# Kernel tuning notes

Hardware: AMD Instinct MI355X
Metric: run time of the kernel (lower is better)

Reference implementation:

```python
import jax, jax.numpy as jnp
import numpy as np

B, T, D, R, DFF = 4, 4096, 1024, 128, 4096
WINDOW = 1024
EPS = 1e-6


def rmsnorm(x, w):
    x32 = x.astype(jnp.float32)
    rms = jax.lax.rsqrt(jnp.mean(x32 * x32, axis=-1, keepdims=True) + EPS)
    return (x32 * rms).astype(x.dtype) * w


def rope(x, cos, sin):
    # x: (B, T, R); cos/sin: (T, R//2)
    d = x.shape[-1] // 2
    x1, x2 = x[..., :d], x[..., d:]
    return jnp.concatenate([x1 * cos + x2 * sin, -x1 * sin + x2 * cos], axis=-1)


def setup_inputs() -> dict:
    key = jax.random.key(0)
    ks = jax.random.split(key, 12)
    s = 0.02  # realistic weight scale
    return {
        "x": jax.random.normal(ks[0], (B, T, D), jnp.float32),
        "Uq": jax.random.normal(ks[1], (R, D), jnp.float32) * s,
        "Uk": jax.random.normal(ks[2], (R, D), jnp.float32) * s,
        "Uv": jax.random.normal(ks[3], (R, D), jnp.float32) * s,
        "cos": jnp.cos(jnp.outer(jnp.arange(T, dtype=jnp.float32),
                                 1.0 / (10000.0 ** (jnp.arange(R // 2, dtype=jnp.float32) / (R // 2))))),
        "sin": jnp.sin(jnp.outer(jnp.arange(T, dtype=jnp.float32),
                                 1.0 / (10000.0 ** (jnp.arange(R // 2, dtype=jnp.float32) / (R // 2))))),
        "ln1_w": jnp.ones((D,), jnp.float32),
        "ln2_w": jnp.ones((D,), jnp.float32),
        "Wo": jax.random.normal(ks[4], (D, R), jnp.float32) * s,
        "w1": jax.random.normal(ks[5], (DFF, D), jnp.float32) * s,
        "w3": jax.random.normal(ks[6], (DFF, D), jnp.float32) * s,
        "w2": jax.random.normal(ks[7], (D, DFF), jnp.float32) * s,
        "window_size": WINDOW,
    }


def reference(x, Uq, Uk, Uv, cos, sin, ln1_w, ln2_w, Wo, w1, w3, w2, window_size):
    Bx, Tx, _ = x.shape
    rank = Uq.shape[0]
    normed = rmsnorm(x, ln1_w)
    q = rope(normed @ Uq.T, cos, sin)  # (B, T, R)
    k = rope(normed @ Uk.T, cos, sin)
    v = normed @ Uv.T
    # windowed causal single-head SDPA
    scale = 1.0 / jnp.sqrt(jnp.float32(rank))
    scores = jnp.einsum("btr,bsr->bts", q, k) * scale  # (B, T, T)
    row = jnp.arange(Tx)[:, None]
    col = jnp.arange(Tx)[None, :]
    mask = (col <= row) & ((row - col) <= window_size)
    scores = jnp.where(mask, scores, jnp.float32(-jnp.inf))
    attn = jax.nn.softmax(scores, axis=-1)
    y = jnp.einsum("bts,bsr->btr", attn, v)  # (B, T, R)
    x = x + y @ Wo.T
    h = rmsnorm(x, ln2_w)
    ffn = ((h @ w1.T) * jax.nn.silu(h @ w3.T)) @ w2.T
    return x + ffn
```

## Files before the change

kernel.cpp:

```cpp
#include <hip/hip_runtime.h>
#include <hip/hip_bf16.h>
#include <stdint.h>

#define BT   16384
#define TT   4096
#define NB   4
#define DD   1024
#define RR   128
#define DFFC 4096

typedef __bf16 bf16_8 __attribute__((ext_vector_type(8)));
typedef float  f32x4  __attribute__((ext_vector_type(4)));

__device__ __forceinline__ void async16(const void* g, void* l) {
  __builtin_amdgcn_global_load_lds((__attribute__((address_space(1))) void*)(g),
                                   (__attribute__((address_space(3))) void*)(l),
                                   16, 0, 0);
}

__global__ __launch_bounds__(256) void cvt_k(const float* __restrict__ src,
                                             __hip_bfloat16* __restrict__ dst, int n4) {
  const int i = blockIdx.x * 256 + threadIdx.x;
  if (i >= n4) return;
  const float4 v = ((const float4*)src)[i];
  __hip_bfloat16* o = dst + (size_t)i * 4;
  o[0] = __float2bfloat16(v.x);
  o[1] = __float2bfloat16(v.y);
  o[2] = __float2bfloat16(v.z);
  o[3] = __float2bfloat16(v.w);
}

__global__ __launch_bounds__(256) void rmsnorm_k(const float* __restrict__ x,
                                                 const float* __restrict__ wgt,
                                                 __hip_bfloat16* __restrict__ out) {
  const int row = blockIdx.x;
  const int t = threadIdx.x;
  const float4 v = ((const float4*)(x + (size_t)row * DD))[t];
  float ss = v.x*v.x + v.y*v.y + v.z*v.z + v.w*v.w;
  #pragma unroll
  for (int m = 1; m < 64; m <<= 1) ss += __shfl_xor(ss, m, 64);
  __shared__ float red[4];
  if ((t & 63) == 0) red[t >> 6] = ss;
  __syncthreads();
  ss = red[0] + red[1] + red[2] + red[3];
  const float rms = rsqrtf(ss * (1.0f / DD) + 1e-6f);
  const float4 wv = ((const float4*)wgt)[t];
  __hip_bfloat16* o = out + (size_t)row * DD + t * 4;
  o[0] = __float2bfloat16(v.x * rms * wv.x);
  o[1] = __float2bfloat16(v.y * rms * wv.y);
  o[2] = __float2bfloat16(v.z * rms * wv.z);
  o[3] = __float2bfloat16(v.w * rms * wv.w);
}

__global__ __launch_bounds__(256) void rope_k(const __hip_bfloat16* __restrict__ qkv,
                                              const float* __restrict__ cosb,
                                              const float* __restrict__ sinb,
                                              __hip_bfloat16* __restrict__ qr,
                                              __hip_bfloat16* __restrict__ kr) {
  const int idx = blockIdx.x * 256 + threadIdx.x;
  const int row = idx >> 6;
  const int i = idx & 63;
  const int tpos = row & (TT - 1);
  const float c = cosb[tpos * 64 + i];
  const float s = sinb[tpos * 64 + i];
  const size_t base = (size_t)row * 384;
  const float q1 = __bfloat162float(qkv[base + i]);
  const float q2 = __bfloat162float(qkv[base + 64 + i]);
  const float k1 = __bfloat162float(qkv[base + 128 + i]);
  const float k2 = __bfloat162float(qkv[base + 192 + i]);
  const size_t ob = (size_t)row * 128;
  qr[ob + i]      = __float2bfloat16( q1 * c + q2 * s);
  qr[ob + 64 + i] = __float2bfloat16(-q1 * s + q2 * c);
  kr[ob + i]      = __float2bfloat16( k1 * c + k2 * s);
  kr[ob + 64 + i] = __float2bfloat16(-k1 * s + k2 * c);
}

__global__ __launch_bounds__(256) void vtrans_k(const __hip_bfloat16* __restrict__ qkv,
                                                __hip_bfloat16* __restrict__ Vt) {
  const int b = blockIdx.y, t0 = blockIdx.x * 64, t = threadIdx.x;
  #pragma unroll
  for (int i = 0; i < 4; ++i) {
    const int flat8 = i * 256 + t;
    const int row = flat8 >> 4;
    const int d8 = (flat8 & 15) * 8;
    const bf16_8 v = *(const bf16_8*)&qkv[((size_t)(b * TT + t0 + row)) * 384 + 256 + d8];
    #pragma unroll
    for (int j = 0; j < 8; ++j)
      ((__bf16*)Vt)[((size_t)(b * 128 + d8 + j)) * TT + t0 + row] = v[j];
  }
}

enum { EPI_BF16 = 0, EPI_RESID = 1, EPI_GATE = 2 };

template <int EPI>
__global__ __launch_bounds__(256) void gemm_bt(
    const __hip_bfloat16* __restrict__ A,
    const __hip_bfloat16* __restrict__ Bw,
    const float* __restrict__ resid,
    const __hip_bfloat16* __restrict__ gate,
    __hip_bfloat16* __restrict__ outb,
    float* __restrict__ outf,
    int N, int K) {
  __shared__ __hip_bfloat16 As[128 * 64];
  __shared__ __hip_bfloat16 Bs[128 * 64];
  const int t = threadIdx.x;
  const int w = t >> 6, lane = t & 63;
  const int wm = w >> 1, wn = w & 1;
  const int quad = lane >> 4, l16 = lane & 15;
  const int m0 = blockIdx.y * 128, n0 = blockIdx.x * 128;

  const __hip_bfloat16* Ab = A + (size_t)m0 * K;
  const __hip_bfloat16* Bb = Bw + (size_t)n0 * K;

  const int rloc = w * 8 + (lane >> 3);
  const int c0 = (((lane & 7) ^ ((lane >> 3) & 7)) << 3);
  const int swz = (l16 & 7);

  f32x4 acc[4][4] = {};

  for (int k0 = 0; k0 < K; k0 += 64) {
    #pragma unroll
    for (int j = 0; j < 4; ++j) {
      async16(Ab + (size_t)(j * 32 + rloc) * K + k0 + c0, &As[j * 2048 + w * 512]);
      async16(Bb + (size_t)(j * 32 + rloc) * K + k0 + c0, &Bs[j * 2048 + w * 512]);
    }
    __syncthreads();
    #pragma unroll
    for (int kc = 0; kc < 2; ++kc) {
      bf16_8 af[4], bfr[4];
      #pragma unroll
      for (int i = 0; i < 4; ++i) {
        const int pos = (((kc * 4 + quad) ^ swz) << 3);
        af[i]  = *(const bf16_8*)&As[(wm * 64 + i * 16 + l16) * 64 + pos];
        bfr[i] = *(const bf16_8*)&Bs[(wn * 64 + i * 16 + l16) * 64 + pos];
      }
      #pragma unroll
      for (int mt = 0; mt < 4; ++mt) {
        #pragma unroll
        for (int nt = 0; nt < 4; ++nt)
          acc[mt][nt] = __builtin_amdgcn_mfma_f32_16x16x32_bf16(af[mt], bfr[nt], acc[mt][nt], 0, 0, 0);
      }
    }
    __syncthreads();
  }

  #pragma unroll
  for (int mt = 0; mt < 4; ++mt) {
    #pragma unroll
    for (int nt = 0; nt < 4; ++nt) {
      #pragma unroll
      for (int r = 0; r < 4; ++r) {
        const int row = m0 + wm * 64 + mt * 16 + quad * 4 + r;
        const int col = n0 + wn * 64 + nt * 16 + l16;
        const size_t idx = (size_t)row * N + col;
        const float v = acc[mt][nt][r];
        if (EPI == EPI_BF16) {
          outb[idx] = __float2bfloat16(v);
        } else if (EPI == EPI_RESID) {
          outf[idx] = resid[idx] + v;
        } else {
          const float sv = v / (1.0f + __expf(-v));
          outb[idx] = __float2bfloat16(__bfloat162float(gate[idx]) * sv);
        }
      }
    }
  }
}

__global__ __launch_bounds__(256) void attn_k(const __hip_bfloat16* __restrict__ qr,
                                              const __hip_bfloat16* __restrict__ kr,
                                              const __hip_bfloat16* __restrict__ Vt,
                                              __hip_bfloat16* __restrict__ y,
                                              const int* __restrict__ winp) {
  __shared__ __hip_bfloat16 Ksm[64 * 128];
  __shared__ __hip_bfloat16 Vsm[128 * 64];
  __shared__ __hip_bfloat16 Psm[4 * 16 * 72];
  const int t = threadIdx.x, w = t >> 6, lane = t & 63;
  const int quad = lane >> 4, l16 = lane & 15;
  const int b = blockIdx.y, t0 = blockIdx.x * 64;
  const int tw0 = t0 + w * 16;
  const int win = *winp;
  int kb_lo = t0 - win;
  if (kb_lo < 0) kb_lo = 0;
  kb_lo &= ~63;

  bf16_8 qf[4];
  const __hip_bfloat16* qb = qr + ((size_t)(b * TT + tw0 + l16)) * 128 + quad * 8;
  #pragma unroll
  for (int kk = 0; kk < 4; ++kk) qf[kk] = *(const bf16_8*)(qb + kk * 32);

  f32x4 o[8] = {};
  float mrow[4] = {-1e30f, -1e30f, -1e30f, -1e30f};
  float lrow[4] = {0.f, 0.f, 0.f, 0.f};
  const float scale = 0.08838834764831845f;

  const int krow_loc = (w * 4) + (lane >> 4);
  const int kc = ((lane & 15) ^ (krow_loc & 15)) << 3;
  const int vloc = lane >> 3;
  const int vc = ((lane & 7) ^ vloc) << 3;

  for (int kb0 = kb_lo; kb0 <= t0; kb0 += 64) {
    const __hip_bfloat16* kbp = kr + ((size_t)(b * TT + kb0)) * 128;
    #pragma unroll
    for (int i = 0; i < 4; ++i) {
      const int krow = i * 16 + krow_loc;
      async16(kbp + (size_t)krow * 128 + kc, &Ksm[i * 2048 + w * 512]);
    }
    #pragma unroll
    for (int i = 0; i < 4; ++i) {
      const int d0 = (i * 4 + w) * 8;
      const int dr = d0 + vloc;
      async16(Vt + ((size_t)(b * 128 + dr)) * TT + kb0 + vc, &Vsm[d0 * 64]);
    }
    __syncthreads();

    f32x4 s[4] = {};
    #pragma unroll
    for (int kk = 0; kk < 4; ++kk) {
      #pragma unroll
      for (int nt = 0; nt < 4; ++nt) {
        const int cc = ((kk * 4 + quad) ^ l16) << 3;
        const bf16_8 bfrag = *(const bf16_8*)&Ksm[(nt * 16 + l16) * 128 + cc];
        s[nt] = __builtin_amdgcn_mfma_f32_16x16x32_bf16(qf[kk], bfrag, s[nt], 0, 0, 0);
      }
    }

    float mb[4] = {-1e30f, -1e30f, -1e30f, -1e30f};
    #pragma unroll
    for (int nt = 0; nt < 4; ++nt) {
      #pragma unroll
      for (int r = 0; r < 4; ++r) {
        const int tq = tw0 + quad * 4 + r;
        const int scol = kb0 + nt * 16 + l16;
        float v = s[nt][r] * scale;
        const bool ok = (scol <= tq) && (tq - scol <= win);
        v = ok ? v : -1e30f;
        s[nt][r] = v;
        mb[r] = fmaxf(mb[r], v);
      }
    }

    #pragma unroll
    for (int r = 0; r < 4; ++r) {
      float m = mb[r];
      m = fmaxf(m, __shfl_xor(m, 1, 16));
      m = fmaxf(m, __shfl_xor(m, 2, 16));
      m = fmaxf(m, __shfl_xor(m, 4, 16));
      m = fmaxf(m, __shfl_xor(m, 8, 16));
      const float mn = fmaxf(mrow[r], m);
      const float alpha = __expf(mrow[r] - mn);
      mrow[r] = mn;
      float rs = 0.f;
      #pragma unroll
      for (int nt = 0; nt < 4; ++nt) {
        const float pv = __expf(s[nt][r] - mn);
        s[nt][r] = pv;
        rs += pv;
      }
      rs += __shfl_xor(rs, 1, 16);
      rs += __shfl_xor(rs, 2, 16);
      rs += __shfl_xor(rs, 4, 16);
      rs += __shfl_xor(rs, 8, 16);
      lrow[r] = lrow[r] * alpha + rs;
      #pragma unroll
      for (int n2 = 0; n2 < 8; ++n2) o[n2][r] *= alpha;
    }

    __hip_bfloat16* pw = &Psm[w * 1152];
    #pragma unroll
    for (int nt = 0; nt < 4; ++nt) {
      #pragma unroll
      for (int r = 0; r < 4; ++r)
        pw[(quad * 4 + r) * 72 + nt * 16 + l16] = __float2bfloat16(s[nt][r]);
    }
    asm volatile("s_waitcnt lgkmcnt(0)" ::: "memory");

    #pragma unroll
    for (int kk2 = 0; kk2 < 2; ++kk2) {
      const bf16_8 pa = *(const bf16_8*)&Psm[w * 1152 + l16 * 72 + kk2 * 32 + quad * 8];
      #pragma unroll
      for (int n2 = 0; n2 < 8; ++n2) {
        const int cc = ((kk2 * 4 + quad) ^ (l16 & 7)) << 3;
        const bf16_8 vb = *(const bf16_8*)&Vsm[(n2 * 16 + l16) * 64 + cc];
        o[n2] = __builtin_amdgcn_mfma_f32_16x16x32_bf16(pa, vb, o[n2], 0, 0, 0);
      }
    }
    __syncthreads();
  }

  #pragma unroll
  for (int n2 = 0; n2 < 8; ++n2) {
    #pragma unroll
    for (int r = 0; r < 4; ++r) {
      const int row = b * TT + tw0 + quad * 4 + r;
      const int col = n2 * 16 + l16;
      y[(size_t)row * 128 + col] = __float2bfloat16(o[n2][r] / lrow[r]);
    }
  }
}

extern "C" void kernel_launch(void* const* d_in, const int* in_sizes, int n_in,
                              void* d_out, int out_size, void* d_ws, size_t ws_size,
                              hipStream_t stream) {
  const float* x    = (const float*)d_in[0];
  const float* Uq   = (const float*)d_in[1];
  const float* Uk   = (const float*)d_in[2];
  const float* Uv   = (const float*)d_in[3];
  const float* cosb = (const float*)d_in[4];
  const float* sinb = (const float*)d_in[5];
  const float* ln1  = (const float*)d_in[6];
  const float* ln2  = (const float*)d_in[7];
  const float* Wo   = (const float*)d_in[8];
  const float* w1   = (const float*)d_in[9];
  const float* w3   = (const float*)d_in[10];
  const float* w2   = (const float*)d_in[11];
  const int*   winp = (const int*)d_in[12];
  float* out = (float*)d_out;

  uint8_t* p = (uint8_t*)d_ws;
  auto take = [&](size_t bytes) {
    uint8_t* q = p;
    p += (bytes + 255) & ~(size_t)255;
    return q;
  };

  __hip_bfloat16* h1     = (__hip_bfloat16*)take((size_t)BT * DFFC * 2);
  __hip_bfloat16* gb     = h1;
  __hip_bfloat16* normed = (__hip_bfloat16*)take((size_t)BT * DD * 2);
  __hip_bfloat16* hb     = normed;
  __hip_bfloat16* qkv    = (__hip_bfloat16*)take((size_t)BT * 384 * 2);
  __hip_bfloat16* yb     = qkv;
  __hip_bfloat16* qr_    = (__hip_bfloat16*)take((size_t)BT * RR * 2);
  __hip_bfloat16* kr_    = (__hip_bfloat16*)take((size_t)BT * RR * 2);
  __hip_bfloat16* Vt     = (__hip_bfloat16*)take((size_t)BT * RR * 2);
  __hip_bfloat16* Ucat   = (__hip_bfloat16*)take((size_t)384 * DD * 2);
  __hip_bfloat16* Wob    = (__hip_bfloat16*)take((size_t)DD * RR * 2);
  __hip_bfloat16* W1b    = (__hip_bfloat16*)take((size_t)DFFC * DD * 2);
  __hip_bfloat16* W3b    = (__hip_bfloat16*)take((size_t)DFFC * DD * 2);
  __hip_bfloat16* W2b    = (__hip_bfloat16*)take((size_t)DD * DFFC * 2);
  float* x_mid = out;

  cvt_k<<<128, 256, 0, stream>>>(Uq, Ucat, RR * DD / 4);
  cvt_k<<<128, 256, 0, stream>>>(Uk, Ucat + (size_t)RR * DD, RR * DD / 4);
  cvt_k<<<128, 256, 0, stream>>>(Uv, Ucat + (size_t)2 * RR * DD, RR * DD / 4);
  cvt_k<<<128, 256, 0, stream>>>(Wo, Wob, DD * RR / 4);
  cvt_k<<<4096, 256, 0, stream>>>(w1, W1b, DFFC * DD / 4);
  cvt_k<<<4096, 256, 0, stream>>>(w3, W3b, DFFC * DD / 4);
  cvt_k<<<4096, 256, 0, stream>>>(w2, W2b, DD * DFFC / 4);

  rmsnorm_k<<<BT, 256, 0, stream>>>(x, ln1, normed);

  gemm_bt<EPI_BF16><<<dim3(3, 128), 256, 0, stream>>>(normed, Ucat, nullptr, nullptr,
                                                      qkv, nullptr, 384, DD);

  rope_k<<<BT * 64 / 256, 256, 0, stream>>>(qkv, cosb, sinb, qr_, kr_);
  vtrans_k<<<dim3(TT / 64, NB), 256, 0, stream>>>(qkv, Vt);

  attn_k<<<dim3(TT / 64, NB), 256, 0, stream>>>(qr_, kr_, Vt, yb, winp);

  gemm_bt<EPI_RESID><<<dim3(8, 128), 256, 0, stream>>>(yb, Wob, x, nullptr,
                                                       nullptr, x_mid, DD, RR);

  rmsnorm_k<<<BT, 256, 0, stream>>>(x_mid, ln2, hb);

  gemm_bt<EPI_BF16><<<dim3(32, 128), 256, 0, stream>>>(hb, W1b, nullptr, nullptr,
                                                       h1, nullptr, DFFC, DD);
  gemm_bt<EPI_GATE><<<dim3(32, 128), 256, 0, stream>>>(hb, W3b, nullptr, h1,
                                                       gb, nullptr, DFFC, DD);
  gemm_bt<EPI_RESID><<<dim3(8, 128), 256, 0, stream>>>(gb, W2b, x_mid, nullptr,
                                                       nullptr, out, DD, DFFC);
}
```

Before: 845.8 us.

## Add 256x256-tile pipelined GEMM kernel for the FFN matmuls

Adds a new 512-thread GEMM kernel with 256x256 output tiles, double-buffered async global-to-LDS loads that are interleaved with MFMA quarter-steps, XOR-swizzled LDS layout, raised wave priority during MFMA, and an XCD-aware block remapping. The three FFN GEMMs now use it in place of the 128x128 kernel. The aim is higher data reuse per tile and better overlap of loads with matrix math on the largest matmuls. In exchange it needs 128 KB of LDS per block and many accumulator registers, which limits occupancy. Its correctness depends on the dimensions dividing evenly by 256.

```diff
diff --git a/kernel.cpp b/kernel.cpp
--- a/kernel.cpp
+++ b/kernel.cpp
@@ -167,6 +167,130 @@
   }
 }
 
+#define G256_BAR()  asm volatile("s_barrier" ::: "memory")
+#define G256_VMW4() asm volatile("s_waitcnt vmcnt(4)" ::: "memory")
+#define G256_VMW0() asm volatile("s_waitcnt vmcnt(0)" ::: "memory")
+
+#define G256_DSA(mh_) \
+  { _Pragma("unroll") for (int mt = 0; mt < 4; ++mt) { \
+      const int rb_ = (rbA + (mh_) * 64 + mt * 16) * 64; \
+      a[mt][0] = *(const bf16_8*)&Ac[rb_ + p0]; \
+      a[mt][1] = *(const bf16_8*)&Ac[rb_ + p1]; } }
+
+#define G256_DSB(nh_) \
+  { _Pragma("unroll") for (int nt = 0; nt < 2; ++nt) { \
+      const int rb_ = (rbB + (nh_) * 32 + nt * 16) * 64; \
+      b[nt][0] = *(const bf16_8*)&Bc[rb_ + p0]; \
+      b[nt][1] = *(const bf16_8*)&Bc[rb_ + p1]; } }
+
+#define G256_MMA(mh_, nh_) \
+  { __builtin_amdgcn_s_setprio(1); \
+    _Pragma("unroll") for (int kk = 0; kk < 2; ++kk) \
+      _Pragma("unroll") for (int mt = 0; mt < 4; ++mt) \
+        _Pragma("unroll") for (int nt = 0; nt < 2; ++nt) \
+          acc[(mh_) * 4 + mt][(nh_) * 2 + nt] = __builtin_amdgcn_mfma_f32_16x16x32_bf16( \
+              a[mt][kk], b[nt][kk], acc[(mh_) * 4 + mt][(nh_) * 2 + nt], 0, 0, 0); \
+    __builtin_amdgcn_s_setprio(0); }
+
+#define G256_TILE(CUR, kt_) { \
+    const __hip_bfloat16* Ac = As[CUR]; \
+    const __hip_bfloat16* Bc = Bs[CUR]; \
+    const int nb_ = (CUR) ^ 1; \
+    const bool pf = ((kt_) + 1) < NT; \
+    const int kn = ((kt_) + 1) << 6; \
+    if (!pf) { G256_VMW0(); G256_BAR(); } \
+    G256_DSA(0); G256_DSB(0); if (pf) { stageA(0, nb_, kn); } \
+    G256_BAR(); G256_MMA(0, 0); G256_VMW4(); G256_BAR(); \
+    G256_DSB(1); if (pf) { stageB(0, nb_, kn); } \
+    G256_BAR(); G256_MMA(0, 1); G256_VMW4(); G256_BAR(); \
+    G256_DSA(1); if (pf) { stageB(1, nb_, kn); } \
+    G256_BAR(); G256_MMA(1, 1); G256_VMW4(); G256_BAR(); \
+    G256_DSB(0); if (pf) { stageA(1, nb_, kn); } \
+    G256_BAR(); G256_MMA(1, 0); G256_VMW4(); G256_BAR(); \
+  }
+
+template <int EPI>
+__global__ __launch_bounds__(512, 2) void gemm256(
+    const __hip_bfloat16* __restrict__ A,
+    const __hip_bfloat16* __restrict__ Bw,
+    const float* __restrict__ resid,
+    const __hip_bfloat16* __restrict__ gate,
+    __hip_bfloat16* __restrict__ outb,
+    float* __restrict__ outf,
+    int N, int K) {
+  __shared__ __hip_bfloat16 As[2][256 * 64];
+  __shared__ __hip_bfloat16 Bs[2][256 * 64];
+  const int t = threadIdx.x;
+  const int w = t >> 6, lane = t & 63;
+  const int wm = w >> 2, wn = w & 3;
+  const int quad = lane >> 4, l16 = lane & 15;
+
+  const int gx = gridDim.x;
+  const int nwg = gx * gridDim.y;
+  int lin = blockIdx.y * gx + blockIdx.x;
+  lin = (lin & 7) * (nwg >> 3) + (lin >> 3);
+  const int m0 = (lin / gx) * 256;
+  const int n0 = (lin % gx) * 256;
+
+  const __hip_bfloat16* Ab = A + (size_t)m0 * K;
+  const __hip_bfloat16* Bb = Bw + (size_t)n0 * K;
+
+  const int rl = lane >> 3;
+  const int c0 = (((lane & 7) ^ rl) << 3);
+
+  auto stageA = [&](int h, int buf, int k0) {
+    const int r0 = h * 64 + (w << 3);
+    async16(Ab + (size_t)(r0 + rl) * K + k0 + c0, &As[buf][r0 * 64]);
+    const int r1 = r0 + 128;
+    async16(Ab + (size_t)(r1 + rl) * K + k0 + c0, &As[buf][r1 * 64]);
+  };
+  auto stageB = [&](int h, int buf, int k0) {
+    const int s0 = (w >> 2) * 64 + h * 32 + (w & 3) * 8;
+    async16(Bb + (size_t)(s0 + rl) * K + k0 + c0, &Bs[buf][s0 * 64]);
+    const int s1 = s0 + 128;
+    async16(Bb + (size_t)(s1 + rl) * K + k0 + c0, &Bs[buf][s1 * 64]);
+  };
+
+  const int rbA = wm * 128 + l16;
+  const int rbB = wn * 64 + l16;
+  const int p0 = ((quad ^ (l16 & 7)) << 3);
+  const int p1 = (((4 + quad) ^ (l16 & 7)) << 3);
+
+  f32x4 acc[8][4] = {};
+  bf16_8 a[4][2], b[2][2];
+  const int NT = K >> 6;
+
+  stageA(0, 0, 0); stageB(0, 0, 0); stageB(1, 0, 0); stageA(1, 0, 0);
+  G256_VMW4(); G256_BAR();
+
+  for (int kt = 0; kt < NT; kt += 2) {
+    G256_TILE(0, kt);
+    G256_TILE(1, kt + 1);
+  }
+
+  #pragma unroll
+  for (int mf = 0; mf < 8; ++mf) {
+    #pragma unroll
+    for (int nf = 0; nf < 4; ++nf) {
+      #pragma unroll
+      for (int r = 0; r < 4; ++r) {
+        const int row = m0 + wm * 128 + mf * 16 + quad * 4 + r;
+        const int col = n0 + wn * 64 + nf * 16 + l16;
+        const size_t idx = (size_t)row * N + col;
+        const float v = acc[mf][nf][r];
+        if (EPI == EPI_BF16) {
+          outb[idx] = __float2bfloat16(v);
+        } else if (EPI == EPI_RESID) {
+          outf[idx] = resid[idx] + v;
+        } else {
+          const float sv = v / (1.0f + __expf(-v));
+          outb[idx] = __float2bfloat16(__bfloat162float(gate[idx]) * sv);
+        }
+      }
+    }
+  }
+}
+
 __global__ __launch_bounds__(256) void attn_k(const __hip_bfloat16* __restrict__ qr,
                                               const __hip_bfloat16* __restrict__ kr,
                                               const __hip_bfloat16* __restrict__ Vt,
@@ -363,10 +487,10 @@
 
   rmsnorm_k<<<BT, 256, 0, stream>>>(x_mid, ln2, hb);
 
-  gemm_bt<EPI_BF16><<<dim3(32, 128), 256, 0, stream>>>(hb, W1b, nullptr, nullptr,
-                                                       h1, nullptr, DFFC, DD);
-  gemm_bt<EPI_GATE><<<dim3(32, 128), 256, 0, stream>>>(hb, W3b, nullptr, h1,
-                                                       gb, nullptr, DFFC, DD);
-  gemm_bt<EPI_RESID><<<dim3(8, 128), 256, 0, stream>>>(gb, W2b, x_mid, nullptr,
-                                                       nullptr, out, DD, DFFC);
-}
+  gemm256<EPI_BF16><<<dim3(16, 64), 512, 0, stream>>>(hb, W1b, nullptr, nullptr,
+                                                      h1, nullptr, DFFC, DD);
+  gemm256<EPI_GATE><<<dim3(16, 64), 512, 0, stream>>>(hb, W3b, nullptr, h1,
+                                                      gb, nullptr, DFFC, DD);
+  gemm256<EPI_RESID><<<dim3(4, 64), 512, 0, stream>>>(gb, W2b, x_mid, nullptr,
+                                                      nullptr, out, DD, DFFC);
+}
```

Result: faster. 754.2 us (-10.8%).
